# Kernel tuning notes

Measured on AMD Instinct MI355X. Metric: run time of the kernel, lower is better.

## Reference

```python
import jax, jax.numpy as jnp
import numpy as np

B, L, D = 8, 2048, 1152  # batch, frames, d_model (multiple of headdim=36)


def setup_inputs() -> dict:
    key = jax.random.key(0)
    k1, k2, k3 = jax.random.split(key, 3)
    hidden_states = jax.random.normal(k1, (B, L, D), dtype=jnp.float32)
    Wq = jax.random.normal(k2, (D, D), dtype=jnp.float32) * 0.02  # xavier-ish, gain 0.1
    Wk = jax.random.normal(k3, (D, D), dtype=jnp.float32) * 0.02
    log_temperature = jnp.zeros((), dtype=jnp.float32)
    boundary_bias = jnp.asarray(-1.0, dtype=jnp.float32)
    mask = jnp.ones((B, L), dtype=bool)
    return dict(hidden_states=hidden_states, Wq=Wq, Wk=Wk,
                log_temperature=log_temperature, boundary_bias=boundary_bias,
                mask=mask)


def _normalize(x, eps=1e-12):
    # F.normalize: x / max(||x||, eps)
    n = jnp.sqrt(jnp.sum(x * x, axis=-1, keepdims=True))
    return x / jnp.maximum(n, eps)


def reference(hidden_states, Wq, Wk, log_temperature, boundary_bias, mask):
    Bb, Ll, Dd = hidden_states.shape
    # ---- RoutingModule (eval mode: argmax boundary decision) ----
    q = jnp.einsum('bld,ed->ble', hidden_states[:, :-1], Wq)
    k = jnp.einsum('bld,ed->ble', hidden_states[:, 1:], Wk)
    cos_sim = jnp.sum(_normalize(q) * _normalize(k), axis=-1)          # (B, L-1)
    temperature = jnp.clip(jnp.exp(log_temperature), 0.1, 10.0)
    bl = (1.0 - cos_sim) * temperature + boundary_bias                 # dissimilarity logits
    bl = jnp.pad(bl, ((0, 0), (1, 0)), constant_values=10.0)           # force boundary at t=0
    logits = jnp.stack([-bl, bl], axis=-1)                             # (B, L, 2)
    boundary_prob = jax.nn.softmax(logits, axis=-1)
    boundary_mask = (bl > 0) & mask                                    # argmax == 1  <=>  bl > 0
    selected_probs = jnp.where(boundary_mask, boundary_prob[..., 1], boundary_prob[..., 0])

    # ---- ChunkLayer: stable-sort boundary frames to the front (static M = L pad) ----
    token_idx = jnp.arange(Ll)[None, :] + (~boundary_mask).astype(jnp.int32) * Ll
    sorted_idx = jnp.argsort(token_idx, axis=1)                        # (B, L)
    chunked = jnp.take_along_axis(hidden_states, sorted_idx[..., None], axis=1)  # (B, L, D)

    # ---- DeChunkLayer: EMA over chunks  h_t = (1-p_t) h_{t-1} + p_t x_t,  h_0 = x_0 ----
    p = jnp.clip(boundary_prob[..., 1], 1e-4, 1.0 - 1e-4)
    p_c = jnp.take_along_axis(p, sorted_idx, axis=1)                   # (B, L)
    a = (1.0 - p_c).at[:, 0].set(0.0)[..., None]                       # (B, L, 1)
    b = (p_c[..., None] * chunked).at[:, 0].set(chunked[:, 0])         # (B, L, D)

    def combine(c1, c2):
        a1, b1 = c1
        a2, b2 = c2
        return a1 * a2, a2 * b1 + b2

    _, ema = jax.lax.associative_scan(combine, (a, b), axis=1)         # (B, L, D)

    # scatter-expand: position t reads chunk (cumsum(boundary) - 1)
    chunk_idx = jnp.clip(jnp.cumsum(boundary_mask.astype(jnp.int32), axis=1) - 1, 0, Ll - 1)
    expanded = jnp.take_along_axis(ema, chunk_idx[..., None], axis=1)  # (B, L, D)

    # STE confidence gate: forward multiplies by 1, backward routes grad to selected_probs
    ste = 1.0 + selected_probs - jax.lax.stop_gradient(selected_probs)
    return expanded * ste[..., None]
```

## Files before the change

kernel.cpp:

```cpp
#include <hip/hip_runtime.h>
#include <hip/hip_bf16.h>
#include <cstdint>
#include <cstddef>

#define Bc 8
#define Lc 2048
#define Dc 1152
#define STRIDE 2080
#define G 8
#define NCHUNK 36

#define WCV_OFF   0u
#define PART_OFF  10616832u
#define BL_OFF    17694720u
#define PV_OFF    17760256u
#define BPOS_OFF  17826816u
#define NB_OFF    17893376u

using bf16x8 = __attribute__((ext_vector_type(8))) short;
using f32x4  = __attribute__((ext_vector_type(4))) float;
#define MFMA(a, b, c) __builtin_amdgcn_mfma_f32_16x16x32_bf16(a, b, c, 0, 0, 0)

__device__ __forceinline__ void gld16(const void* g, void* l) {
    __builtin_amdgcn_global_load_lds(
        (const __attribute__((address_space(1))) void*)(g),
        (__attribute__((address_space(3))) void*)(l), 16, 0, 0);
}

__device__ __forceinline__ unsigned short bf_hi(float x) {
    __hip_bfloat16 h = __float2bfloat16(x);
    return *reinterpret_cast<unsigned short*>(&h);
}
__device__ __forceinline__ float bf_f(unsigned short u) {
    __hip_bfloat16 h; *reinterpret_cast<unsigned short*>(&h) = u;
    return __bfloat162float(h);
}

__global__ __launch_bounds__(256) void k0_convert(
    const float* __restrict__ H, const float* __restrict__ Wq,
    const float* __restrict__ Wk, char* __restrict__ Hcv, char* __restrict__ Wcv)
{
    int idx = blockIdx.x * 256 + threadIdx.x;
    if (idx >= (16384 + 2304) * 144) return;
    int cchunk = idx & 3;
    int ks = (idx >> 2) % 36;
    int row = idx / 144;
    const float* src;
    char* dst;
    if (row < 16384) {
        src = H + (size_t)row * Dc;
        dst = Hcv + ((size_t)row * 36 + ks) * 128;
    } else {
        int e = row - 16384;
        src = (e < Dc) ? (Wq + (size_t)e * Dc) : (Wk + (size_t)(e - Dc) * Dc);
        dst = Wcv + ((size_t)e * 36 + ks) * 128;
    }
    const float* s = src + ks * 32 + cchunk * 8;
    unsigned int hw0 = 0, hw1 = 0, hw2 = 0, hw3 = 0;
    unsigned int lw0 = 0, lw1 = 0, lw2 = 0, lw3 = 0;
    #define CV(i, HW, LW, SH)                                                  \
    {                                                                          \
        float x = s[i];                                                        \
        unsigned short h = bf_hi(x);                                           \
        unsigned short lo = bf_hi(x - bf_f(h));                                \
        HW |= ((unsigned int)h) << (SH);                                       \
        LW |= ((unsigned int)lo) << (SH);                                      \
    }
    CV(0, hw0, lw0, 0) CV(1, hw0, lw0, 16) CV(2, hw1, lw1, 0) CV(3, hw1, lw1, 16)
    CV(4, hw2, lw2, 0) CV(5, hw2, lw2, 16) CV(6, hw3, lw3, 0) CV(7, hw3, lw3, 16)
    #undef CV
    uint4 hv; hv.x = hw0; hv.y = hw1; hv.z = hw2; hv.w = hw3;
    uint4 lv; lv.x = lw0; lv.y = lw1; lv.z = lw2; lv.w = lw3;
    *(uint4*)(dst + cchunk * 16) = hv;
    *(uint4*)(dst + 64 + cchunk * 16) = lv;
}

__global__ __launch_bounds__(256, 2) void k1_mfma(
    const char* __restrict__ Hcv, const char* __restrict__ Wcv,
    float* __restrict__ partial)
{
    __shared__ __align__(16) char LdsB[24704];
    const int tid = threadIdx.x;
    const int bx = blockIdx.x;
    const int j = blockIdx.y;
    const int batch = bx >> 4;
    const int mt = bx & 15;
    const int t0 = 1 + mt * 128;
    const int rowbase = batch * Lc + t0 - 1;
    const int rowmax = batch * Lc + (Lc - 1);

    const int l = tid & 63;
    const int w = tid >> 6;
    const int rl = l & 15;
    const int c = l >> 4;

    const int offA = rl * 128 + ((c ^ ((rl >> 1) & 3)) << 4);
    const int offB = (rl + 1) * 128 + ((c ^ (((rl + 1) >> 1) & 3)) << 4);
    const char* Hb = LdsB;
    const char* Wb = LdsB + 16512;

    f32x4 q00 = {0.f,0.f,0.f,0.f}, q01 = {0.f,0.f,0.f,0.f};
    f32x4 q10 = {0.f,0.f,0.f,0.f}, q11 = {0.f,0.f,0.f,0.f};
    f32x4 k00 = {0.f,0.f,0.f,0.f}, k01 = {0.f,0.f,0.f,0.f};
    f32x4 k10 = {0.f,0.f,0.f,0.f}, k11 = {0.f,0.f,0.f,0.f};

    for (int ks = 0; ks < 36; ++ks) {
        for (int u = tid; u < 1032; u += 256) {
            int row = u >> 3;
            int p = (u >> 2) & 1;
            int ch = (u & 3) ^ ((row >> 1) & 3);
            int grow = rowbase + row; if (grow > rowmax) grow = rowmax;
            gld16(Hcv + ((size_t)grow * 36 + ks) * 128 + p * 64 + ch * 16,
                  LdsB + u * 16);
        }
        for (int u = tid; u < 512; u += 256) {
            int row = u >> 3;
            int p = (u >> 2) & 1;
            int ch = (u & 3) ^ ((row >> 1) & 3);
            int erow = (row < 32) ? (j * 32 + row) : (Dc + j * 32 + row - 32);
            gld16(Wcv + ((size_t)erow * 36 + ks) * 128 + p * 64 + ch * 16,
                  LdsB + 16512 + u * 16);
        }
        __syncthreads();

        bf16x8 wq0h = *(const bf16x8*)(Wb + offA);
        bf16x8 wq0l = *(const bf16x8*)(Wb + offA + 64);
        bf16x8 wq1h = *(const bf16x8*)(Wb + 2048 + offA);
        bf16x8 wq1l = *(const bf16x8*)(Wb + 2048 + offA + 64);
        bf16x8 wk0h = *(const bf16x8*)(Wb + 4096 + offA);
        bf16x8 wk0l = *(const bf16x8*)(Wb + 4096 + offA + 64);
        bf16x8 wk1h = *(const bf16x8*)(Wb + 6144 + offA);
        bf16x8 wk1l = *(const bf16x8*)(Wb + 6144 + offA + 64);
        {
            const char* hm = Hb + (2 * w) * 2048;
            bf16x8 ah = *(const bf16x8*)(hm + offA);
            bf16x8 al = *(const bf16x8*)(hm + offA + 64);
            bf16x8 bh = *(const bf16x8*)(hm + offB);
            bf16x8 bl = *(const bf16x8*)(hm + offB + 64);
            q00 = MFMA(ah, wq0h, q00); q00 = MFMA(ah, wq0l, q00); q00 = MFMA(al, wq0h, q00);
            q01 = MFMA(ah, wq1h, q01); q01 = MFMA(ah, wq1l, q01); q01 = MFMA(al, wq1h, q01);
            k00 = MFMA(bh, wk0h, k00); k00 = MFMA(bh, wk0l, k00); k00 = MFMA(bl, wk0h, k00);
            k01 = MFMA(bh, wk1h, k01); k01 = MFMA(bh, wk1l, k01); k01 = MFMA(bl, wk1h, k01);
        }
        {
            const char* hm = Hb + (2 * w + 1) * 2048;
            bf16x8 ah = *(const bf16x8*)(hm + offA);
            bf16x8 al = *(const bf16x8*)(hm + offA + 64);
            bf16x8 bh = *(const bf16x8*)(hm + offB);
            bf16x8 bl = *(const bf16x8*)(hm + offB + 64);
            q10 = MFMA(ah, wq0h, q10); q10 = MFMA(ah, wq0l, q10); q10 = MFMA(al, wq0h, q10);
            q11 = MFMA(ah, wq1h, q11); q11 = MFMA(ah, wq1l, q11); q11 = MFMA(al, wq1h, q11);
            k10 = MFMA(bh, wk0h, k10); k10 = MFMA(bh, wk0l, k10); k10 = MFMA(bl, wk0h, k10);
            k11 = MFMA(bh, wk1h, k11); k11 = MFMA(bh, wk1l, k11); k11 = MFMA(bl, wk1h, k11);
        }
        __syncthreads();
    }

    #define EMIT(QA, QB, KA, KB, TROW)                                         \
    {                                                                          \
        float qq = (QA) * (QA) + (QB) * (QB);                                  \
        float kk = (KA) * (KA) + (KB) * (KB);                                  \
        float qk = (QA) * (KA) + (QB) * (KB);                                  \
        qq += __shfl_xor(qq, 1, 64); qq += __shfl_xor(qq, 2, 64);              \
        qq += __shfl_xor(qq, 4, 64); qq += __shfl_xor(qq, 8, 64);              \
        kk += __shfl_xor(kk, 1, 64); kk += __shfl_xor(kk, 2, 64);              \
        kk += __shfl_xor(kk, 4, 64); kk += __shfl_xor(kk, 8, 64);              \
        qk += __shfl_xor(qk, 1, 64); qk += __shfl_xor(qk, 2, 64);              \
        qk += __shfl_xor(qk, 4, 64); qk += __shfl_xor(qk, 8, 64);              \
        if (rl == 0) {                                                         \
            int t = t0 + (TROW);                                               \
            if (t < Lc) {                                                      \
                size_t pidx = (((size_t)j * Bc + batch) * Lc + t) * 3;         \
                partial[pidx] = qq; partial[pidx + 1] = kk;                    \
                partial[pidx + 2] = qk;                                        \
            }                                                                  \
        }                                                                      \
    }
    EMIT(q00[0], q01[0], k00[0], k01[0], 32 * w + c * 4 + 0)
    EMIT(q00[1], q01[1], k00[1], k01[1], 32 * w + c * 4 + 1)
    EMIT(q00[2], q01[2], k00[2], k01[2], 32 * w + c * 4 + 2)
    EMIT(q00[3], q01[3], k00[3], k01[3], 32 * w + c * 4 + 3)
    EMIT(q10[0], q11[0], k10[0], k11[0], 32 * w + 16 + c * 4 + 0)
    EMIT(q10[1], q11[1], k10[1], k11[1], 32 * w + 16 + c * 4 + 1)
    EMIT(q10[2], q11[2], k10[2], k11[2], 32 * w + 16 + c * 4 + 2)
    EMIT(q10[3], q11[3], k10[3], k11[3], 32 * w + 16 + c * 4 + 3)
    #undef EMIT
}

__global__ __launch_bounds__(256) void k1b_reduce(
    const float* __restrict__ partial, const float* __restrict__ ltemp,
    const float* __restrict__ bbias, float* __restrict__ bl_out)
{
    int idx = blockIdx.x * 256 + threadIdx.x;
    if (idx >= Bc * Lc) return;
    int t = idx & (Lc - 1);
    if (t == 0) return;
    float qq = 0.f, kk = 0.f, qk = 0.f;
    #pragma unroll
    for (int cn = 0; cn < NCHUNK; ++cn) {
        size_t p = ((size_t)cn * Bc * Lc + idx) * 3;
        qq += partial[p];
        kk += partial[p + 1];
        qk += partial[p + 2];
    }
    float T = expf(ltemp[0]);
    T = fminf(fmaxf(T, 0.1f), 10.0f);
    float den = fmaxf(sqrtf(qq), 1e-12f) * fmaxf(sqrtf(kk), 1e-12f);
    bl_out[idx] = (1.0f - qk / den) * T + bbias[0];
}

__global__ __launch_bounds__(256) void k2_boundary(
    const float* __restrict__ bl_in, const int* __restrict__ mask,
    float* __restrict__ pv, int* __restrict__ bpos, int* __restrict__ nb)
{
    int b = blockIdx.x;
    int tid = threadIdx.x;
    const float* blb = bl_in + b * Lc;
    const int* mb = mask + b * Lc;

    float blv[8]; int f[8];
    int t0 = tid * 8;
    int s = 0;
    #pragma unroll
    for (int i = 0; i < 8; ++i) {
        int t = t0 + i;
        float v = (t == 0) ? 10.0f : blb[t];
        blv[i] = v;
        f[i] = (v > 0.0f && mb[t] != 0) ? 1 : 0;
        s += f[i];
    }
    int lane = tid & 63, wv = tid >> 6;
    int sc = s;
    #pragma unroll
    for (int off = 1; off < 64; off <<= 1) {
        int o = __shfl_up(sc, off, 64);
        if (lane >= off) sc += o;
    }
    __shared__ int wsums[4];
    if (lane == 63) wsums[wv] = sc;
    __syncthreads();
    int woff = 0;
    #pragma unroll
    for (int w2 = 0; w2 < 4; ++w2) woff += (w2 < wv) ? wsums[w2] : 0;
    int excl = woff + sc - s;
    int total = wsums[0] + wsums[1] + wsums[2] + wsums[3];

    float* pvb = pv + b * STRIDE;
    int* bpb = bpos + b * STRIDE;
    int r = excl;
    #pragma unroll
    for (int i = 0; i < 8; ++i) {
        if (f[i]) {
            int t = t0 + i;
            float p;
            if (t == 0) {
                p = 1.0f;
            } else {
                p = 1.0f / (1.0f + expf(-2.0f * blv[i]));
                p = fminf(fmaxf(p, 1e-4f), 1.0f - 1e-4f);
            }
            bpb[r] = t;
            pvb[r] = p;
            r += 1;
        }
    }
    if (tid == 0) nb[b] = total;
    for (int q = total + tid; q < STRIDE; q += 256) { bpb[q] = Lc; pvb[q] = 0.0f; }
}

__global__ __launch_bounds__(128) void k3_ema(
    const float* __restrict__ H, const float* __restrict__ pv,
    const int* __restrict__ bpos, const int* __restrict__ nb,
    float* __restrict__ out)
{
    int b = blockIdx.x;
    int ch = blockIdx.y * 128 + threadIdx.x;
    const float* Hb = H + (size_t)b * Lc * Dc + ch;
    float* Ob = out + (size_t)b * Lc * Dc + ch;
    const float* pvb = pv + b * STRIDE;
    const int* bpb = bpos + b * STRIDE;
    int n = nb[b];
    int ng = (n + G - 1) / G;

    float xA[G], pA[G]; int tA[G + 1];
    #pragma unroll
    for (int i = 0; i < G; ++i) {
        int t = bpb[i];
        tA[i] = t;
        pA[i] = pvb[i];
        xA[i] = (t < Lc) ? Hb[(size_t)t * Dc] : 0.0f;
    }
    tA[G] = bpb[G];

    float h = 0.0f;
    for (int g = 0; g < ng; ++g) {
        int nbase = (g + 1) * G;
        float xB[G], pB[G]; int tB[G + 1];
        #pragma unroll
        for (int i = 0; i < G; ++i) {
            int t = bpb[nbase + i];
            tB[i] = t;
            pB[i] = pvb[nbase + i];
            xB[i] = (t < Lc) ? Hb[(size_t)t * Dc] : 0.0f;
        }
        tB[G] = bpb[nbase + G];
        #pragma unroll
        for (int i = 0; i < G; ++i) {
            h = (1.0f - pA[i]) * h + pA[i] * xA[i];
            int te = tA[i + 1];
            for (int tt = tA[i]; tt < te; ++tt) Ob[(size_t)tt * Dc] = h;
        }
        #pragma unroll
        for (int i = 0; i < G; ++i) { xA[i] = xB[i]; pA[i] = pB[i]; tA[i] = tB[i]; }
        tA[G] = tB[G];
    }
}

extern "C" void kernel_launch(void* const* d_in, const int* in_sizes, int n_in,
                              void* d_out, int out_size, void* d_ws, size_t ws_size,
                              hipStream_t stream)
{
    const float* H  = (const float*)d_in[0];
    const float* Wq = (const float*)d_in[1];
    const float* Wk = (const float*)d_in[2];
    const float* lt = (const float*)d_in[3];
    const float* bb = (const float*)d_in[4];
    const int* mask = (const int*)d_in[5];
    float* out = (float*)d_out;

    char* ws = (char*)d_ws;
    char*  Hcv  = (char*)d_out;
    char*  Wcv  = ws + WCV_OFF;
    float* part = (float*)(ws + PART_OFF);
    float* bl   = (float*)(ws + BL_OFF);
    float* pv   = (float*)(ws + PV_OFF);
    int*   bpos = (int*)(ws + BPOS_OFF);
    int*   nbp  = (int*)(ws + NB_OFF);

    hipLaunchKernelGGL(k0_convert, dim3(((16384 + 2304) * 144 + 255) / 256),
                       dim3(256), 0, stream, H, Wq, Wk, Hcv, Wcv);
    hipLaunchKernelGGL(k1_mfma, dim3(Bc * 16, NCHUNK), dim3(256), 0, stream,
                       Hcv, Wcv, part);
    hipLaunchKernelGGL(k1b_reduce, dim3((Bc * Lc + 255) / 256), dim3(256), 0, stream,
                       part, lt, bb, bl);
    hipLaunchKernelGGL(k2_boundary, dim3(Bc), dim3(256), 0, stream,
                       bl, mask, pv, bpos, nbp);
    hipLaunchKernelGGL(k3_ema, dim3(Bc, 9), dim3(128), 0, stream,
                       H, pv, bpos, nbp, out);
}
```

Measured before the change: 436.4 us.

## Swap k1 grid order, hoist load pointers, and change LDS swizzle to 3-bit XOR

The MFMA projection kernel now uses the 36 output-column chunks as blockIdx.x, so consecutive blocks share the same H row tile and can reuse it in L2. Global-to-LDS load addresses are computed once before the k-loop and advanced by 128 bytes per step, removing per-iteration index math and loop overhead. The LDS swizzle changes from a 2-bit XOR over half-rows to a 3-bit XOR across all eight 16-byte chunks, with the low half located via XOR 4, to reduce bank conflicts. The per-step stride of 128 bytes implies the converted layout's row stride is unchanged, so correctness depends on the new swizzle matching the read offsets.

```diff
diff --git a/kernel.cpp b/kernel.cpp
--- a/kernel.cpp
+++ b/kernel.cpp
@@ -81,21 +81,48 @@
 {
     __shared__ __align__(16) char LdsB[24704];
     const int tid = threadIdx.x;
-    const int bx = blockIdx.x;
-    const int j = blockIdx.y;
+    const int j = blockIdx.x;
+    const int bx = blockIdx.y;
     const int batch = bx >> 4;
     const int mt = bx & 15;
     const int t0 = 1 + mt * 128;
     const int rowbase = batch * Lc + t0 - 1;
     const int rowmax = batch * Lc + (Lc - 1);
 
+    const char *hp0, *hp1, *hp2, *hp3, *hpt, *wp0, *wp1;
+    {
+        #define HP(P, U)                                                       \
+        {                                                                      \
+            int u = (U); int row = u >> 3;                                     \
+            int ch = (u & 7) ^ (row & 7);                                      \
+            int grow = rowbase + row; if (grow > rowmax) grow = rowmax;        \
+            P = Hcv + (size_t)grow * 4608 + (ch << 4);                         \
+        }
+        HP(hp0, tid) HP(hp1, tid + 256) HP(hp2, tid + 512) HP(hp3, tid + 768)
+        HP(hpt, 1024 + (tid & 7))
+        #undef HP
+        #define WP(P, U)                                                       \
+        {                                                                      \
+            int u = (U); int row = u >> 3;                                     \
+            int ch = (u & 7) ^ (row & 7);                                      \
+            int erow = (row < 32) ? (j * 32 + row) : (Dc + j * 32 + row - 32); \
+            P = Wcv + (size_t)erow * 4608 + (ch << 4);                         \
+        }
+        WP(wp0, tid) WP(wp1, tid + 256)
+        #undef WP
+    }
+
     const int l = tid & 63;
     const int w = tid >> 6;
     const int rl = l & 15;
     const int c = l >> 4;
 
-    const int offA = rl * 128 + ((c ^ ((rl >> 1) & 3)) << 4);
-    const int offB = (rl + 1) * 128 + ((c ^ (((rl + 1) >> 1) & 3)) << 4);
+    const int sA = c ^ (rl & 7);
+    const int sB = c ^ ((rl + 1) & 7);
+    const int offAh = rl * 128 + (sA << 4);
+    const int offAl = rl * 128 + ((sA ^ 4) << 4);
+    const int offBh = (rl + 1) * 128 + (sB << 4);
+    const int offBl = (rl + 1) * 128 + ((sB ^ 4) << 4);
     const char* Hb = LdsB;
     const char* Wb = LdsB + 16512;
 
@@ -105,38 +132,31 @@
     f32x4 k10 = {0.f,0.f,0.f,0.f}, k11 = {0.f,0.f,0.f,0.f};
 
     for (int ks = 0; ks < 36; ++ks) {
-        for (int u = tid; u < 1032; u += 256) {
-            int row = u >> 3;
-            int p = (u >> 2) & 1;
-            int ch = (u & 3) ^ ((row >> 1) & 3);
-            int grow = rowbase + row; if (grow > rowmax) grow = rowmax;
-            gld16(Hcv + ((size_t)grow * 36 + ks) * 128 + p * 64 + ch * 16,
-                  LdsB + u * 16);
-        }
-        for (int u = tid; u < 512; u += 256) {
-            int row = u >> 3;
-            int p = (u >> 2) & 1;
-            int ch = (u & 3) ^ ((row >> 1) & 3);
-            int erow = (row < 32) ? (j * 32 + row) : (Dc + j * 32 + row - 32);
-            gld16(Wcv + ((size_t)erow * 36 + ks) * 128 + p * 64 + ch * 16,
-                  LdsB + 16512 + u * 16);
-        }
+        gld16(hp0, LdsB + tid * 16);
+        gld16(hp1, LdsB + (tid + 256) * 16);
+        gld16(hp2, LdsB + (tid + 512) * 16);
+        gld16(hp3, LdsB + (tid + 768) * 16);
+        if (tid < 8) gld16(hpt, LdsB + (1024 + tid) * 16);
+        gld16(wp0, LdsB + 16512 + tid * 16);
+        gld16(wp1, LdsB + 16512 + (tid + 256) * 16);
+        hp0 += 128; hp1 += 128; hp2 += 128; hp3 += 128; hpt += 128;
+        wp0 += 128; wp1 += 128;
         __syncthreads();
 
-        bf16x8 wq0h = *(const bf16x8*)(Wb + offA);
-        bf16x8 wq0l = *(const bf16x8*)(Wb + offA + 64);
-        bf16x8 wq1h = *(const bf16x8*)(Wb + 2048 + offA);
-        bf16x8 wq1l = *(const bf16x8*)(Wb + 2048 + offA + 64);
-        bf16x8 wk0h = *(const bf16x8*)(Wb + 4096 + offA);
-        bf16x8 wk0l = *(const bf16x8*)(Wb + 4096 + offA + 64);
-        bf16x8 wk1h = *(const bf16x8*)(Wb + 6144 + offA);
-        bf16x8 wk1l = *(const bf16x8*)(Wb + 6144 + offA + 64);
+        bf16x8 wq0h = *(const bf16x8*)(Wb + offAh);
+        bf16x8 wq0l = *(const bf16x8*)(Wb + offAl);
+        bf16x8 wq1h = *(const bf16x8*)(Wb + 2048 + offAh);
+        bf16x8 wq1l = *(const bf16x8*)(Wb + 2048 + offAl);
+        bf16x8 wk0h = *(const bf16x8*)(Wb + 4096 + offAh);
+        bf16x8 wk0l = *(const bf16x8*)(Wb + 4096 + offAl);
+        bf16x8 wk1h = *(const bf16x8*)(Wb + 6144 + offAh);
+        bf16x8 wk1l = *(const bf16x8*)(Wb + 6144 + offAl);
         {
             const char* hm = Hb + (2 * w) * 2048;
-            bf16x8 ah = *(const bf16x8*)(hm + offA);
-            bf16x8 al = *(const bf16x8*)(hm + offA + 64);
-            bf16x8 bh = *(const bf16x8*)(hm + offB);
-            bf16x8 bl = *(const bf16x8*)(hm + offB + 64);
+            bf16x8 ah = *(const bf16x8*)(hm + offAh);
+            bf16x8 al = *(const bf16x8*)(hm + offAl);
+            bf16x8 bh = *(const bf16x8*)(hm + offBh);
+            bf16x8 bl = *(const bf16x8*)(hm + offBl);
             q00 = MFMA(ah, wq0h, q00); q00 = MFMA(ah, wq0l, q00); q00 = MFMA(al, wq0h, q00);
             q01 = MFMA(ah, wq1h, q01); q01 = MFMA(ah, wq1l, q01); q01 = MFMA(al, wq1h, q01);
             k00 = MFMA(bh, wk0h, k00); k00 = MFMA(bh, wk0l, k00); k00 = MFMA(bl, wk0h, k00);
@@ -144,10 +164,10 @@
         }
         {
             const char* hm = Hb + (2 * w + 1) * 2048;
-            bf16x8 ah = *(const bf16x8*)(hm + offA);
-            bf16x8 al = *(const bf16x8*)(hm + offA + 64);
-            bf16x8 bh = *(const bf16x8*)(hm + offB);
-            bf16x8 bl = *(const bf16x8*)(hm + offB + 64);
+            bf16x8 ah = *(const bf16x8*)(hm + offAh);
+            bf16x8 al = *(const bf16x8*)(hm + offAl);
+            bf16x8 bh = *(const bf16x8*)(hm + offBh);
+            bf16x8 bl = *(const bf16x8*)(hm + offBl);
             q10 = MFMA(ah, wq0h, q10); q10 = MFMA(ah, wq0l, q10); q10 = MFMA(al, wq0h, q10);
             q11 = MFMA(ah, wq1h, q11); q11 = MFMA(ah, wq1l, q11); q11 = MFMA(al, wq1h, q11);
             k10 = MFMA(bh, wk0h, k10); k10 = MFMA(bh, wk0l, k10); k10 = MFMA(bl, wk0h, k10);
@@ -339,7 +359,7 @@
 
     hipLaunchKernelGGL(k0_convert, dim3(((16384 + 2304) * 144 + 255) / 256),
                        dim3(256), 0, stream, H, Wq, Wk, Hcv, Wcv);
-    hipLaunchKernelGGL(k1_mfma, dim3(Bc * 16, NCHUNK), dim3(256), 0, stream,
+    hipLaunchKernelGGL(k1_mfma, dim3(NCHUNK, Bc * 16), dim3(256), 0, stream,
                        Hcv, Wcv, part);
     hipLaunchKernelGGL(k1b_reduce, dim3((Bc * Lc + 255) / 256), dim3(256), 0, stream,
                        part, lt, bb, bl);
```

After: 404.9 us. 7.2% less time.

## Widen GEMM N-tile to 64 columns per block and halve partial chunks

Applied to the files above, without the earlier changes.

Each k1 block now computes 64 output columns of Q and K instead of 32. The H tile loaded into LDS is therefore reused across twice as many weight columns, and the grid shrinks from 36 to 18 column chunks. This also halves the partial buffer that the reduce kernel sums. The LDS layout changes to a full-row XOR swizzle with precomputed pointers, block IDs are remapped so neighbouring blocks share weight tiles, and sched_barriers are added between MFMA groups. The cost is more accumulator registers and more LDS per block, which may reduce occupancy.

```diff
diff --git a/kernel.cpp b/kernel.cpp
--- a/kernel.cpp
+++ b/kernel.cpp
@@ -8,7 +8,7 @@
 #define Dc 1152
 #define STRIDE 2080
 #define G 8
-#define NCHUNK 36
+#define NCHUNK 18
 
 #define WCV_OFF   0u
 #define PART_OFF  10616832u
@@ -79,88 +79,102 @@
     const char* __restrict__ Hcv, const char* __restrict__ Wcv,
     float* __restrict__ partial)
 {
-    __shared__ __align__(16) char LdsB[24704];
+    __shared__ __align__(16) char LdsB[32896];
     const int tid = threadIdx.x;
-    const int bx = blockIdx.x;
-    const int j = blockIdx.y;
-    const int batch = bx >> 4;
-    const int mt = bx & 15;
+    const int bid = blockIdx.x;
+    const int x = bid & 7;
+    const int r = bid >> 3;
+    const int g = x + 8 * (r / 18);
+    const int j = r % 18;
+    const int batch = g >> 4;
+    const int mt = g & 15;
     const int t0 = 1 + mt * 128;
     const int rowbase = batch * Lc + t0 - 1;
     const int rowmax = batch * Lc + (Lc - 1);
+
+    const char *hp0, *hpt, *wp0;
+    {
+        int row = tid >> 3;
+        int ch = (tid & 7) ^ (row & 7);
+        hp0 = Hcv + (size_t)(rowbase + row) * 4608 + (ch << 4);
+        int gr2 = rowbase + 128; if (gr2 > rowmax) gr2 = rowmax;
+        hpt = Hcv + (size_t)gr2 * 4608 + ((tid & 7) << 4);
+        wp0 = Wcv + (size_t)(j * 64 + row) * 4608 + (ch << 4);
+    }
 
     const int l = tid & 63;
     const int w = tid >> 6;
     const int rl = l & 15;
     const int c = l >> 4;
 
-    const int offA = rl * 128 + ((c ^ ((rl >> 1) & 3)) << 4);
-    const int offB = (rl + 1) * 128 + ((c ^ (((rl + 1) >> 1) & 3)) << 4);
-    const char* Hb = LdsB;
+    const int sA = c ^ (rl & 7);
+    const int sB = c ^ ((rl + 1) & 7);
+    const int offAh = rl * 128 + (sA << 4);
+    const int offAl = rl * 128 + ((sA ^ 4) << 4);
+    const int offBh = (rl + 1) * 128 + (sB << 4);
+    const int offBl = (rl + 1) * 128 + ((sB ^ 4) << 4);
     const char* Wb = LdsB + 16512;
 
-    f32x4 q00 = {0.f,0.f,0.f,0.f}, q01 = {0.f,0.f,0.f,0.f};
-    f32x4 q10 = {0.f,0.f,0.f,0.f}, q11 = {0.f,0.f,0.f,0.f};
-    f32x4 k00 = {0.f,0.f,0.f,0.f}, k01 = {0.f,0.f,0.f,0.f};
-    f32x4 k10 = {0.f,0.f,0.f,0.f}, k11 = {0.f,0.f,0.f,0.f};
+    f32x4 q00{0,0,0,0}, q01{0,0,0,0}, q02{0,0,0,0}, q03{0,0,0,0};
+    f32x4 q10{0,0,0,0}, q11{0,0,0,0}, q12{0,0,0,0}, q13{0,0,0,0};
+    f32x4 k00{0,0,0,0}, k01{0,0,0,0}, k02{0,0,0,0}, k03{0,0,0,0};
+    f32x4 k10{0,0,0,0}, k11{0,0,0,0}, k12{0,0,0,0}, k13{0,0,0,0};
 
     for (int ks = 0; ks < 36; ++ks) {
-        for (int u = tid; u < 1032; u += 256) {
-            int row = u >> 3;
-            int p = (u >> 2) & 1;
-            int ch = (u & 3) ^ ((row >> 1) & 3);
-            int grow = rowbase + row; if (grow > rowmax) grow = rowmax;
-            gld16(Hcv + ((size_t)grow * 36 + ks) * 128 + p * 64 + ch * 16,
-                  LdsB + u * 16);
+        gld16(hp0,           LdsB + tid * 16);
+        gld16(hp0 + 147456,  LdsB + (tid + 256) * 16);
+        gld16(hp0 + 294912,  LdsB + (tid + 512) * 16);
+        gld16(hp0 + 442368,  LdsB + (tid + 768) * 16);
+        if (tid < 8) gld16(hpt, LdsB + (1024 + tid) * 16);
+        gld16(wp0,           LdsB + 16512 + tid * 16);
+        gld16(wp0 + 147456,  LdsB + 16512 + (tid + 256) * 16);
+        gld16(wp0 + 5308416, LdsB + 16512 + (tid + 512) * 16);
+        gld16(wp0 + 5455872, LdsB + 16512 + (tid + 768) * 16);
+        hp0 += 128; hpt += 128; wp0 += 128;
+        __syncthreads();
+
+        const char* hm0 = LdsB + (2 * w) * 2048;
+        const char* hm1 = LdsB + (2 * w + 1) * 2048;
+        bf16x8 a0h = *(const bf16x8*)(hm0 + offAh);
+        bf16x8 a0l = *(const bf16x8*)(hm0 + offAl);
+        bf16x8 b0h = *(const bf16x8*)(hm0 + offBh);
+        bf16x8 b0l = *(const bf16x8*)(hm0 + offBl);
+        bf16x8 a1h = *(const bf16x8*)(hm1 + offAh);
+        bf16x8 a1l = *(const bf16x8*)(hm1 + offAl);
+        bf16x8 b1h = *(const bf16x8*)(hm1 + offBh);
+        bf16x8 b1l = *(const bf16x8*)(hm1 + offBl);
+
+        #define FSTEP(f, QA0, QA1, KA0, KA1)                                   \
+        {                                                                      \
+            const char* wqb = Wb + (f) * 2048;                                 \
+            bf16x8 wh = *(const bf16x8*)(wqb + offAh);                         \
+            bf16x8 wl = *(const bf16x8*)(wqb + offAl);                         \
+            QA0 = MFMA(a0h, wh, QA0); QA0 = MFMA(a0h, wl, QA0);                \
+            QA0 = MFMA(a0l, wh, QA0);                                          \
+            QA1 = MFMA(a1h, wh, QA1); QA1 = MFMA(a1h, wl, QA1);                \
+            QA1 = MFMA(a1l, wh, QA1);                                          \
+            const char* wkb = Wb + 8192 + (f) * 2048;                          \
+            bf16x8 vh = *(const bf16x8*)(wkb + offAh);                         \
+            bf16x8 vl = *(const bf16x8*)(wkb + offAl);                         \
+            KA0 = MFMA(b0h, vh, KA0); KA0 = MFMA(b0h, vl, KA0);                \
+            KA0 = MFMA(b0l, vh, KA0);                                          \
+            KA1 = MFMA(b1h, vh, KA1); KA1 = MFMA(b1h, vl, KA1);                \
+            KA1 = MFMA(b1l, vh, KA1);                                          \
+            __builtin_amdgcn_sched_barrier(0);                                 \
         }
-        for (int u = tid; u < 512; u += 256) {
-            int row = u >> 3;
-            int p = (u >> 2) & 1;
-            int ch = (u & 3) ^ ((row >> 1) & 3);
-            int erow = (row < 32) ? (j * 32 + row) : (Dc + j * 32 + row - 32);
-            gld16(Wcv + ((size_t)erow * 36 + ks) * 128 + p * 64 + ch * 16,
-                  LdsB + 16512 + u * 16);
-        }
+        FSTEP(0, q00, q10, k00, k10)
+        FSTEP(1, q01, q11, k01, k11)
+        FSTEP(2, q02, q12, k02, k12)
+        FSTEP(3, q03, q13, k03, k13)
+        #undef FSTEP
         __syncthreads();
-
-        bf16x8 wq0h = *(const bf16x8*)(Wb + offA);
-        bf16x8 wq0l = *(const bf16x8*)(Wb + offA + 64);
-        bf16x8 wq1h = *(const bf16x8*)(Wb + 2048 + offA);
-        bf16x8 wq1l = *(const bf16x8*)(Wb + 2048 + offA + 64);
-        bf16x8 wk0h = *(const bf16x8*)(Wb + 4096 + offA);
-        bf16x8 wk0l = *(const bf16x8*)(Wb + 4096 + offA + 64);
-        bf16x8 wk1h = *(const bf16x8*)(Wb + 6144 + offA);
-        bf16x8 wk1l = *(const bf16x8*)(Wb + 6144 + offA + 64);
-        {
-            const char* hm = Hb + (2 * w) * 2048;
-            bf16x8 ah = *(const bf16x8*)(hm + offA);
-            bf16x8 al = *(const bf16x8*)(hm + offA + 64);
-            bf16x8 bh = *(const bf16x8*)(hm + offB);
-            bf16x8 bl = *(const bf16x8*)(hm + offB + 64);
-            q00 = MFMA(ah, wq0h, q00); q00 = MFMA(ah, wq0l, q00); q00 = MFMA(al, wq0h, q00);
-            q01 = MFMA(ah, wq1h, q01); q01 = MFMA(ah, wq1l, q01); q01 = MFMA(al, wq1h, q01);
-            k00 = MFMA(bh, wk0h, k00); k00 = MFMA(bh, wk0l, k00); k00 = MFMA(bl, wk0h, k00);
-            k01 = MFMA(bh, wk1h, k01); k01 = MFMA(bh, wk1l, k01); k01 = MFMA(bl, wk1h, k01);
-        }
-        {
-            const char* hm = Hb + (2 * w + 1) * 2048;
-            bf16x8 ah = *(const bf16x8*)(hm + offA);
-            bf16x8 al = *(const bf16x8*)(hm + offA + 64);
-            bf16x8 bh = *(const bf16x8*)(hm + offB);
-            bf16x8 bl = *(const bf16x8*)(hm + offB + 64);
-            q10 = MFMA(ah, wq0h, q10); q10 = MFMA(ah, wq0l, q10); q10 = MFMA(al, wq0h, q10);
-            q11 = MFMA(ah, wq1h, q11); q11 = MFMA(ah, wq1l, q11); q11 = MFMA(al, wq1h, q11);
-            k10 = MFMA(bh, wk0h, k10); k10 = MFMA(bh, wk0l, k10); k10 = MFMA(bl, wk0h, k10);
-            k11 = MFMA(bh, wk1h, k11); k11 = MFMA(bh, wk1l, k11); k11 = MFMA(bl, wk1h, k11);
-        }
-        __syncthreads();
-    }
-
-    #define EMIT(QA, QB, KA, KB, TROW)                                         \
+    }
+
+    #define EMIT(QA, QB, QC, QD, KA, KB, KC, KD, TROW)                         \
     {                                                                          \
-        float qq = (QA) * (QA) + (QB) * (QB);                                  \
-        float kk = (KA) * (KA) + (KB) * (KB);                                  \
-        float qk = (QA) * (KA) + (QB) * (KB);                                  \
+        float qq = (QA)*(QA) + (QB)*(QB) + (QC)*(QC) + (QD)*(QD);              \
+        float kk = (KA)*(KA) + (KB)*(KB) + (KC)*(KC) + (KD)*(KD);              \
+        float qk = (QA)*(KA) + (QB)*(KB) + (QC)*(KC) + (QD)*(KD);              \
         qq += __shfl_xor(qq, 1, 64); qq += __shfl_xor(qq, 2, 64);              \
         qq += __shfl_xor(qq, 4, 64); qq += __shfl_xor(qq, 8, 64);              \
         kk += __shfl_xor(kk, 1, 64); kk += __shfl_xor(kk, 2, 64);              \
@@ -176,14 +190,14 @@
             }                                                                  \
         }                                                                      \
     }
-    EMIT(q00[0], q01[0], k00[0], k01[0], 32 * w + c * 4 + 0)
-    EMIT(q00[1], q01[1], k00[1], k01[1], 32 * w + c * 4 + 1)
-    EMIT(q00[2], q01[2], k00[2], k01[2], 32 * w + c * 4 + 2)
-    EMIT(q00[3], q01[3], k00[3], k01[3], 32 * w + c * 4 + 3)
-    EMIT(q10[0], q11[0], k10[0], k11[0], 32 * w + 16 + c * 4 + 0)
-    EMIT(q10[1], q11[1], k10[1], k11[1], 32 * w + 16 + c * 4 + 1)
-    EMIT(q10[2], q11[2], k10[2], k11[2], 32 * w + 16 + c * 4 + 2)
-    EMIT(q10[3], q11[3], k10[3], k11[3], 32 * w + 16 + c * 4 + 3)
+    EMIT(q00[0], q01[0], q02[0], q03[0], k00[0], k01[0], k02[0], k03[0], 32*w + c*4 + 0)
+    EMIT(q00[1], q01[1], q02[1], q03[1], k00[1], k01[1], k02[1], k03[1], 32*w + c*4 + 1)
+    EMIT(q00[2], q01[2], q02[2], q03[2], k00[2], k01[2], k02[2], k03[2], 32*w + c*4 + 2)
+    EMIT(q00[3], q01[3], q02[3], q03[3], k00[3], k01[3], k02[3], k03[3], 32*w + c*4 + 3)
+    EMIT(q10[0], q11[0], q12[0], q13[0], k10[0], k11[0], k12[0], k13[0], 32*w + 16 + c*4 + 0)
+    EMIT(q10[1], q11[1], q12[1], q13[1], k10[1], k11[1], k12[1], k13[1], 32*w + 16 + c*4 + 1)
+    EMIT(q10[2], q11[2], q12[2], q13[2], k10[2], k11[2], k12[2], k13[2], 32*w + 16 + c*4 + 2)
+    EMIT(q10[3], q11[3], q12[3], q13[3], k10[3], k11[3], k12[3], k13[3], 32*w + 16 + c*4 + 3)
     #undef EMIT
 }
 
@@ -339,7 +353,7 @@
 
     hipLaunchKernelGGL(k0_convert, dim3(((16384 + 2304) * 144 + 255) / 256),
                        dim3(256), 0, stream, H, Wq, Wk, Hcv, Wcv);
-    hipLaunchKernelGGL(k1_mfma, dim3(Bc * 16, NCHUNK), dim3(256), 0, stream,
+    hipLaunchKernelGGL(k1_mfma, dim3(NCHUNK * 128), dim3(256), 0, stream,
                        Hcv, Wcv, part);
     hipLaunchKernelGGL(k1b_reduce, dim3((Bc * Lc + 255) / 256), dim3(256), 0, stream,
                        part, lt, bb, bl);
```

Result: faster. 364.9 us (-16.4%).
